# Optimization experiments

Measured on AMD Instinct MI355X. Metric: run time of the kernel, lower is better.

## Reference

```python
import jax, jax.numpy as jnp
import numpy as np

N = 48
K = 16
COLS = N - K  # 32
B = 65536
FEAT = K * COLS + COLS * COLS + K * K + min(K, COLS)  # 1808


def setup_inputs() -> dict:
    key = jax.random.key(0)
    ks = jax.random.split(key, 9)
    def lin(kw, fan_in, fan_out):
        bound = 1.0 / np.sqrt(fan_in)
        return jax.random.uniform(kw, (fan_in, fan_out), jnp.float32, -bound, bound)
    x = jax.random.normal(ks[0], (B, K * COLS), dtype=jnp.float32)
    W1 = lin(ks[1], FEAT, 256); b1 = jnp.zeros((256,), jnp.float32)
    W2 = lin(ks[2], 256, 128);  b2 = jnp.zeros((128,), jnp.float32)
    W3 = lin(ks[3], 128, 64);   b3 = jnp.zeros((64,), jnp.float32)
    W4 = lin(ks[4], 64, 1);     b4 = jnp.zeros((1,), jnp.float32)
    return {"x": x, "W1": W1, "b1": b1, "W2": W2, "b2": b2,
            "W3": W3, "b3": b3, "W4": W4, "b4": b4}


def reference(x, W1, b1, W2, b2, W3, b3, W4, b4):
    Bn = x.shape[0]
    P = x.reshape(Bn, K, COLS)                      # [B,k,cols]
    gram_cols = jnp.einsum('bki,bkj->bij', P, P)    # P^T P, [B,cols,cols]
    gram_rows = jnp.einsum('bik,bjk->bij', P, P)    # P P^T, [B,k,k]
    svd_vals = jnp.linalg.svd(P, compute_uv=False)  # [B,min(k,cols)]
    feats = jnp.concatenate([
        x,
        gram_cols.reshape(Bn, -1),
        gram_rows.reshape(Bn, -1),
        svd_vals,
    ], axis=1)                                       # [B,1808]
    h = jax.nn.relu(feats @ W1 + b1)
    h = jax.nn.relu(h @ W2 + b2)
    h = jax.nn.relu(h @ W3 + b3)
    return h @ W4 + b4                               # [B,1]
```

## Files before the change

### kernel.cpp

```cpp
#include <hip/hip_runtime.h>
#include <hip/hip_bf16.h>
#include <cstdint>
#include <cstddef>

typedef unsigned short u16;
typedef unsigned int u32;
typedef short short8 __attribute__((ext_vector_type(8)));
typedef short short4v __attribute__((ext_vector_type(4)));
typedef __bf16 bf16x8 __attribute__((ext_vector_type(8)));
typedef float v4f __attribute__((ext_vector_type(4)));
typedef float v16f __attribute__((ext_vector_type(16)));

#define NSAMP 65536
#define FEAT_PAD 1824


__device__ __forceinline__ u16 f2bf(float f) {
  union { float f; u32 u; } v; v.f = f;
  u32 r = (v.u + 0x7FFFu + ((v.u >> 16) & 1u)) >> 16;
  return (u16)r;
}
__device__ __forceinline__ float bf2f(u16 h) {
  union { u32 u; float f; } v; v.u = ((u32)h) << 16;
  return v.f;
}

__device__ __forceinline__ v4f mfma16(short8 a, short8 b, v4f c) {
  return __builtin_amdgcn_mfma_f32_16x16x32_bf16(
      __builtin_bit_cast(bf16x8, a), __builtin_bit_cast(bf16x8, b), c, 0, 0, 0);
}
__device__ __forceinline__ v16f mfma32(short8 a, short8 b, v16f c) {
  return __builtin_amdgcn_mfma_f32_32x32x16_bf16(
      __builtin_bit_cast(bf16x8, a), __builtin_bit_cast(bf16x8, b), c, 0, 0, 0);
}

typedef __attribute__((address_space(1))) const void* gas_ptr;
typedef __attribute__((address_space(3))) void* las_ptr;
__device__ __forceinline__ void gl_lds16(const void* g, void* l) {
  __builtin_amdgcn_global_load_lds((gas_ptr)g, (las_ptr)l, 16, 0, 0);
}

__global__ void prep_kernel(const float* __restrict__ W1, const float* __restrict__ W2,
                            const float* __restrict__ W3,
                            u16* __restrict__ w1t, u16* __restrict__ w2t, u16* __restrict__ w3t) {
  int idx = blockIdx.x * 256 + threadIdx.x;
  if (idx < 256 * FEAT_PAD) {
    int n = idx / FEAT_PAD, kp = idx % FEAT_PAD;
    int k;
    if (kp < 512) {
      k = kp;
    } else if (kp < 1536) {
      int t = kp - 512, ln = t >> 4, rr = t & 15;
      int jj = ln & 31, q2 = ln >> 5;
      int i = (rr & 3) + 8 * (rr >> 2) + 4 * q2;
      k = 512 + i * 32 + jj;
    } else if (kp < 1792) {
      int t = kp - 1536, ln = t >> 2, rr = t & 3;
      int jj = ln & 15;
      int i = (ln >> 4) * 4 + rr;
      k = 1536 + i * 16 + jj;
    } else {
      k = kp;
    }
    size_t addr = (size_t)(n >> 4) * 29184 + (kp >> 3) * 128 + (n & 15) * 8 + (kp & 7);
    w1t[addr] = (kp < 1808) ? f2bf(W1[(size_t)k * 256 + n]) : (u16)0;
  }
  if (idx < 128 * 256) {
    int n = idx / 256, k = idx % 256;
    size_t addr = (size_t)(n >> 4) * 4096 + (k >> 3) * 128 + (n & 15) * 8 + (k & 7);
    w2t[addr] = f2bf(W2[k * 128 + n]);
  }
  if (idx < 64 * 128) {
    int n = idx / 128, k = idx % 128;
    size_t addr = (size_t)(n >> 4) * 2048 + (k >> 3) * 128 + (n & 15) * 8 + (k & 7);
    w3t[addr] = f2bf(W3[k * 64 + n]);
  }
}

__device__ __forceinline__ void svd4(const v4f* aR, u16* tb, int s0, int lane) {
  const int j = lane & 15, bse = lane & 48, q = lane >> 4;
  float a[16];
#pragma unroll
  for (int gi = 0; gi < 4; ++gi)
#pragma unroll
    for (int r = 0; r < 4; ++r) {
      float t0 = __shfl(aR[0][r], gi * 16 + j);
      float t1 = __shfl(aR[1][r], gi * 16 + j);
      float t2 = __shfl(aR[2][r], gi * 16 + j);
      float t3 = __shfl(aR[3][r], gi * 16 + j);
      a[gi * 4 + r] = (q == 0) ? t0 : (q == 1) ? t1 : (q == 2) ? t2 : t3;
    }

  float es[16];
#pragma unroll
  for (int i = 0; i < 16; ++i) es[i] = 0.f;

#pragma unroll
  for (int step = 0; step < 14; ++step) {
    const int i = 15 - step, l = i - 1;
    float xv = a[i];
    float xm = (j <= l) ? xv : 0.f;
    float h = xm * xm;
    h += __shfl_xor(h, 1); h += __shfl_xor(h, 2);
    h += __shfl_xor(h, 4); h += __shfl_xor(h, 8);
    float ul = __shfl(xm, bse + l);
    float sq = sqrtf(h);
    float alpha = (ul >= 0.f) ? -sq : sq;
    float denom = h - ul * alpha;
    float beta = (h > 1e-30f) ? (1.0f / denom) : 0.f;
    float v = (j < l) ? xm : ((j == l) ? (xm - alpha) : 0.f);
    float vv[16], pp[16];
#pragma unroll
    for (int m = 0; m < 16; ++m) vv[m] = (m < i) ? __shfl(v, bse + m) : 0.f;
    float p = 0.f;
#pragma unroll
    for (int m = 0; m < 16; ++m) if (m < i) p = fmaf(a[m], vv[m], p);
    p *= beta;
#pragma unroll
    for (int m = 0; m < 16; ++m) pp[m] = (m <= i) ? __shfl(p, bse + m) : 0.f;
    float Ks = 0.f;
#pragma unroll
    for (int m = 0; m < 16; ++m) if (m < i) Ks = fmaf(pp[m], vv[m], Ks);
    Ks *= 0.5f * beta;
    float wsc = p - Ks * v;
#pragma unroll
    for (int m = 0; m <= 15; ++m) {
      if (m <= i) {
        float wm = pp[m] - Ks * vv[m];
        a[m] -= vv[m] * wsc + wm * v;
      }
    }
    es[i] = alpha;
  }
  es[1] = __shfl(a[1], bse + 0);

  float dsel = a[0];
#pragma unroll
  for (int m = 1; m < 16; ++m) dsel = (j == m) ? a[m] : dsel;
  float dd[16];
#pragma unroll
  for (int m = 0; m < 16; ++m) dd[m] = __shfl(dsel, bse + m);
  float e2a[16];
  e2a[0] = 0.f;
#pragma unroll
  for (int k = 1; k < 16; ++k) e2a[k] = es[k] * es[k] + 1e-30f;
  float dmax = dd[0], emax = 0.f;
#pragma unroll
  for (int m = 1; m < 16; ++m) dmax = fmaxf(dmax, dd[m]);
#pragma unroll
  for (int k = 1; k < 16; ++k) emax = fmaxf(emax, fabsf(es[k]));
  float lo = 0.f, hi = dmax + 2.f * emax + 1e-6f;
#pragma unroll 1
  for (int iter = 0; iter < 15; ++iter) {
    float mid = 0.5f * (lo + hi);
    float qq = dd[0] - mid;
    int cnt = (qq < 0.f) ? 1 : 0;
#pragma unroll
    for (int k = 1; k < 16; ++k) {
      qq = dd[k] - mid - e2a[k] * __builtin_amdgcn_rcpf(qq);
      cnt += (qq < 0.f) ? 1 : 0;
    }
    if (cnt > j) hi = mid; else lo = mid;
  }
  float lam = 0.5f * (lo + hi);
  int t = 15 - j;
  int s = s0 + q;
  tb[(size_t)(224 + (t >> 3)) * 128 + (s & 15) * 8 + (t & 7)] = f2bf(sqrtf(fmaxf(lam, 0.f)));
}

__global__ __launch_bounds__(256) void feat_kernel(const float* __restrict__ x,
                                                   u16* __restrict__ feats) {
  const int lane = threadIdx.x & 63;
  const int wv = threadIdx.x >> 6;
  const int wid = blockIdx.x;
  const int l15 = lane & 15, l31 = lane & 31, q4 = lane >> 4, q2 = lane >> 5;
  const int pbase = l15 * 32 + q4 * 8;
  u16* tb = feats + (size_t)wid * 29184;

  short8 sx[4], sc0[4], sc1[4];
  short4v sr4[4];
  v4f aR[4];
#pragma unroll
  for (int r8 = 0; r8 < 4; ++r8) {
    const int s = wid * 16 + wv * 4 + r8;
    const float* xs = x + (size_t)s * 512;
    float4 p0 = *(const float4*)(xs + pbase);
    float4 p1 = *(const float4*)(xs + pbase + 4);
    float t[8];
#pragma unroll
    for (int j = 0; j < 8; ++j) t[j] = xs[(q2 * 8 + j) * 32 + l31];

    short8 fp, ft;
    fp[0] = (short)f2bf(p0.x); fp[1] = (short)f2bf(p0.y);
    fp[2] = (short)f2bf(p0.z); fp[3] = (short)f2bf(p0.w);
    fp[4] = (short)f2bf(p1.x); fp[5] = (short)f2bf(p1.y);
    fp[6] = (short)f2bf(p1.z); fp[7] = (short)f2bf(p1.w);
#pragma unroll
    for (int j = 0; j < 8; ++j) ft[j] = (short)f2bf(t[j]);

    v4f accR; v16f accC;
#pragma unroll
    for (int r = 0; r < 4; ++r) accR[r] = 0.f;
#pragma unroll
    for (int r = 0; r < 16; ++r) accC[r] = 0.f;
    accR = mfma16(fp, fp, accR);
    accC = mfma32(ft, ft, accC);

    sx[r8] = fp;
#pragma unroll
    for (int r = 0; r < 8; ++r) { sc0[r8][r] = (short)f2bf(accC[r]); sc1[r8][r] = (short)f2bf(accC[r + 8]); }
#pragma unroll
    for (int r = 0; r < 4; ++r) sr4[r8][r] = (short)f2bf(accR[r]);
    aR[r8] = accR;
  }

  const int ho = wv * 4;
#pragma unroll
  for (int r8 = 0; r8 < 4; ++r8)
    *(short8*)(tb + (l15 * 4 + q4) * 128 + (ho + r8) * 8) = sx[r8];
#pragma unroll
  for (int r8 = 0; r8 < 4; ++r8)
    *(short8*)(tb + (64 + lane * 2) * 128 + (ho + r8) * 8) = sc0[r8];
#pragma unroll
  for (int r8 = 0; r8 < 4; ++r8)
    *(short8*)(tb + (65 + lane * 2) * 128 + (ho + r8) * 8) = sc1[r8];
#pragma unroll
  for (int r8 = 0; r8 < 4; ++r8)
    *(short4v*)(tb + (192 + (lane >> 1)) * 128 + (lane & 1) * 4 + (ho + r8) * 8) = sr4[r8];

  if (wv == 3 && lane < 32) {
    short8 z;
#pragma unroll
    for (int j = 0; j < 8; ++j) z[j] = 0;
    *(short8*)(tb + 226 * 128 + lane * 8) = z;
  }

  svd4(aR, tb, wid * 16 + ho, lane);
}

__global__ __launch_bounds__(256, 2) void gemm1_kernel(const u16* __restrict__ feats,
                                                       const u16* __restrict__ w1t,
                                                       const float* __restrict__ b1,
                                                       u16* __restrict__ h1) {
  __shared__ __align__(16) u16 At[8 * 512];
  __shared__ __align__(16) u16 Bt[16 * 512];
  const int tid = threadIdx.x, lane = tid & 63, wv = tid >> 6;
  const int l15 = lane & 15, q4 = lane >> 4;
  const int m0 = blockIdx.x * 128;
  const int wm = (wv & 1) * 64, wn = (wv >> 1) * 128;

  const u16* gA[2]; u16* lA[2];
#pragma unroll
  for (int j = 0; j < 2; ++j) {
    int i = wv * 2 + j;
    gA[j] = feats + (size_t)((m0 >> 4) + i) * 29184 + lane * 8;
    lA[j] = At + i * 512;
  }
  const u16* gB[4]; u16* lB[4];
#pragma unroll
  for (int j = 0; j < 4; ++j) {
    int i = wv * 4 + j;
    gB[j] = w1t + (size_t)i * 29184 + lane * 8;
    lB[j] = Bt + i * 512;
  }

  v4f acc[4][8];
#pragma unroll
  for (int mt = 0; mt < 4; ++mt)
#pragma unroll
    for (int nt = 0; nt < 8; ++nt)
#pragma unroll
      for (int r = 0; r < 4; ++r) acc[mt][nt][r] = 0.f;

  for (int k0 = 0; k0 < FEAT_PAD; k0 += 32) {
    const int go = (k0 >> 3) * 128;
#pragma unroll
    for (int j = 0; j < 2; ++j) gl_lds16(gA[j] + go, lA[j]);
#pragma unroll
    for (int j = 0; j < 4; ++j) gl_lds16(gB[j] + go, lB[j]);
    __syncthreads();

    short8 af[4], bfr[8];
#pragma unroll
    for (int mt = 0; mt < 4; ++mt)
      af[mt] = *(const short8*)(At + ((wv & 1) * 4 + mt) * 512 + q4 * 128 + l15 * 8);
#pragma unroll
    for (int nt = 0; nt < 8; ++nt)
      bfr[nt] = *(const short8*)(Bt + ((wv >> 1) * 8 + nt) * 512 + q4 * 128 + l15 * 8);
#pragma unroll
    for (int mt = 0; mt < 4; ++mt)
#pragma unroll
      for (int nt = 0; nt < 8; ++nt)
        acc[mt][nt] = mfma16(af[mt], bfr[nt], acc[mt][nt]);
    __syncthreads();
  }

#pragma unroll
  for (int mt = 0; mt < 4; ++mt)
#pragma unroll
    for (int nt = 0; nt < 8; ++nt) {
      int col = wn + nt * 16 + l15;
      float bias = b1[col];
#pragma unroll
      for (int r = 0; r < 4; ++r) {
        int row = m0 + wm + mt * 16 + q4 * 4 + r;
        h1[(size_t)row * 256 + col] = f2bf(fmaxf(acc[mt][nt][r] + bias, 0.f));
      }
    }
}

__global__ __launch_bounds__(256, 2) void gemm23_kernel(
    const u16* __restrict__ h1, const u16* __restrict__ w2t, const float* __restrict__ b2,
    const u16* __restrict__ w3t, const float* __restrict__ b3,
    const float* __restrict__ w4, const float* __restrict__ b4, float* __restrict__ out) {
  __shared__ __align__(16) u16 H2[128 * 136];
  const int tid = threadIdx.x, lane = tid & 63, wv = tid >> 6;
  const int l15 = lane & 15, q4 = lane >> 4;
  const int m0 = blockIdx.x * 128;

  const u16* pA[2];
#pragma unroll
  for (int mt = 0; mt < 2; ++mt)
    pA[mt] = h1 + (size_t)(m0 + wv * 32 + mt * 16 + l15) * 256 + q4 * 8;
  const u16* pB[8];
#pragma unroll
  for (int nt = 0; nt < 8; ++nt)
    pB[nt] = w2t + (size_t)nt * 4096 + q4 * 128 + l15 * 8;

  v4f acc[2][8];
#pragma unroll
  for (int mt = 0; mt < 2; ++mt)
#pragma unroll
    for (int nt = 0; nt < 8; ++nt)
#pragma unroll
      for (int r = 0; r < 4; ++r) acc[mt][nt][r] = 0.f;

#pragma unroll
  for (int kk = 0; kk < 8; ++kk) {
    short8 af[2], bfr[8];
#pragma unroll
    for (int mt = 0; mt < 2; ++mt) af[mt] = *(const short8*)(pA[mt] + kk * 32);
#pragma unroll
    for (int nt = 0; nt < 8; ++nt) bfr[nt] = *(const short8*)(pB[nt] + kk * 512);
#pragma unroll
    for (int mt = 0; mt < 2; ++mt)
#pragma unroll
      for (int nt = 0; nt < 8; ++nt)
        acc[mt][nt] = mfma16(af[mt], bfr[nt], acc[mt][nt]);
  }

#pragma unroll
  for (int mt = 0; mt < 2; ++mt)
#pragma unroll
    for (int nt = 0; nt < 8; ++nt) {
      int c = nt * 16 + l15;
      float bias = b2[c];
#pragma unroll
      for (int r = 0; r < 4; ++r) {
        int rl = wv * 32 + mt * 16 + q4 * 4 + r;
        H2[rl * 136 + c] = f2bf(fmaxf(acc[mt][nt][r] + bias, 0.f));
      }
    }

  v4f acc2[2][4];
#pragma unroll
  for (int mt = 0; mt < 2; ++mt)
#pragma unroll
    for (int nt = 0; nt < 4; ++nt)
#pragma unroll
      for (int r = 0; r < 4; ++r) acc2[mt][nt][r] = 0.f;
#pragma unroll
  for (int kk = 0; kk < 4; ++kk) {
    short8 af2[2], bf2v[4];
#pragma unroll
    for (int mt = 0; mt < 2; ++mt)
      af2[mt] = *(const short8*)(H2 + (wv * 32 + mt * 16 + l15) * 136 + kk * 32 + q4 * 8);
#pragma unroll
    for (int nt = 0; nt < 4; ++nt)
      bf2v[nt] = *(const short8*)(w3t + (size_t)nt * 2048 + (kk * 4 + q4) * 128 + l15 * 8);
#pragma unroll
    for (int mt = 0; mt < 2; ++mt)
#pragma unroll
      for (int nt = 0; nt < 4; ++nt)
        acc2[mt][nt] = mfma16(af2[mt], bf2v[nt], acc2[mt][nt]);
  }

  float b4v = b4[0];
#pragma unroll
  for (int mt = 0; mt < 2; ++mt)
#pragma unroll
    for (int r = 0; r < 4; ++r) {
      float p = 0.f;
#pragma unroll
      for (int nt = 0; nt < 4; ++nt) {
        int c = nt * 16 + l15;
        float h3 = fmaxf(acc2[mt][nt][r] + b3[c], 0.f);
        p += h3 * w4[c];
      }
      p += __shfl_xor(p, 1);
      p += __shfl_xor(p, 2);
      p += __shfl_xor(p, 4);
      p += __shfl_xor(p, 8);
      if (l15 == 0) {
        int row = m0 + wv * 32 + mt * 16 + q4 * 4 + r;
        out[row] = p + b4v;
      }
    }
}

extern "C" void kernel_launch(void* const* d_in, const int* in_sizes, int n_in,
                              void* d_out, int out_size, void* d_ws, size_t ws_size,
                              hipStream_t stream) {
  const float* x  = (const float*)d_in[0];
  const float* W1 = (const float*)d_in[1];
  const float* b1 = (const float*)d_in[2];
  const float* W2 = (const float*)d_in[3];
  const float* b2 = (const float*)d_in[4];
  const float* W3 = (const float*)d_in[5];
  const float* b3 = (const float*)d_in[6];
  const float* W4 = (const float*)d_in[7];
  const float* b4 = (const float*)d_in[8];
  float* out = (float*)d_out;

  char* ws = (char*)d_ws;
  u16* feats = (u16*)ws;
  u16* h1    = (u16*)(ws + 239075328ull);
  u16* w1t   = (u16*)(ws + 239075328ull + 33554432ull);
  u16* w2t   = (u16*)(ws + 239075328ull + 33554432ull + 933888ull);
  u16* w3t   = (u16*)(ws + 239075328ull + 33554432ull + 933888ull + 65536ull);

  prep_kernel<<<1824, 256, 0, stream>>>(W1, W2, W3, w1t, w2t, w3t);
  feat_kernel<<<4096, 256, 0, stream>>>(x, feats);
  gemm1_kernel<<<512, 256, 0, stream>>>(feats, w1t, b1, h1);
  gemm23_kernel<<<512, 256, 0, stream>>>(h1, w2t, b2, w3t, b3, W4, b4, out);
}
```

Baseline: 419.2 us.

## Fuse layer-1 GEMM with layers 2-4 via shared-memory h1 staging

Merges gemm1 and gemm23 into a single mlp_kernel. The ReLU'd layer-1 output is written to shared memory in two 64-row halves and consumed in place by the layer-2/3/4 MFMAs, so the 32 MB bf16 h1 round-trip through global memory and one kernel launch go away. Shared memory per block grows to about 50 KB, which may limit occupancy. The extra barriers and serial half loop also leave the accumulator registers live during the tail.

```diff
diff --git a/kernel.cpp b/kernel.cpp
--- a/kernel.cpp
+++ b/kernel.cpp
@@ -238,12 +238,17 @@
   svd4(aR, tb, wid * 16 + ho, lane);
 }
 
-__global__ __launch_bounds__(256, 2) void gemm1_kernel(const u16* __restrict__ feats,
-                                                       const u16* __restrict__ w1t,
-                                                       const float* __restrict__ b1,
-                                                       u16* __restrict__ h1) {
-  __shared__ __align__(16) u16 At[8 * 512];
-  __shared__ __align__(16) u16 Bt[16 * 512];
+__global__ __launch_bounds__(256, 2) void mlp_kernel(
+    const u16* __restrict__ feats, const u16* __restrict__ w1t, const float* __restrict__ b1,
+    const u16* __restrict__ w2t, const float* __restrict__ b2,
+    const u16* __restrict__ w3t, const float* __restrict__ b3,
+    const float* __restrict__ w4, const float* __restrict__ b4, float* __restrict__ out) {
+  __shared__ __align__(16) char sm[51200];
+  u16* At  = (u16*)sm;
+  u16* Bt  = (u16*)(sm + 8192);
+  u16* h1s = (u16*)sm;
+  u16* H2  = (u16*)(sm + 33792);
+
   const int tid = threadIdx.x, lane = tid & 63, wv = tid >> 6;
   const int l15 = lane & 15, q4 = lane >> 4;
   const int m0 = blockIdx.x * 128;
@@ -295,106 +300,71 @@
     __syncthreads();
   }
 
-#pragma unroll
-  for (int mt = 0; mt < 4; ++mt)
-#pragma unroll
-    for (int nt = 0; nt < 8; ++nt) {
-      int col = wn + nt * 16 + l15;
-      float bias = b1[col];
-#pragma unroll
-      for (int r = 0; r < 4; ++r) {
-        int row = m0 + wm + mt * 16 + q4 * 4 + r;
-        h1[(size_t)row * 256 + col] = f2bf(fmaxf(acc[mt][nt][r] + bias, 0.f));
+  const float b4v = b4[0];
+#pragma unroll 1
+  for (int h = 0; h < 2; ++h) {
+    __syncthreads();
+    if ((wv & 1) == h) {
+#pragma unroll
+      for (int mt = 0; mt < 4; ++mt)
+#pragma unroll
+        for (int nt = 0; nt < 8; ++nt) {
+          int col = wn + nt * 16 + l15;
+          float bias = b1[col];
+#pragma unroll
+          for (int r = 0; r < 4; ++r)
+            h1s[(mt * 16 + q4 * 4 + r) * 264 + col] = f2bf(fmaxf(acc[mt][nt][r] + bias, 0.f));
+        }
+    }
+    __syncthreads();
+
+    v4f a2[8];
+#pragma unroll
+    for (int nt = 0; nt < 8; ++nt)
+#pragma unroll
+      for (int r = 0; r < 4; ++r) a2[nt][r] = 0.f;
+#pragma unroll
+    for (int kk = 0; kk < 8; ++kk) {
+      short8 af2 = *(const short8*)(h1s + (wv * 16 + l15) * 264 + kk * 32 + q4 * 8);
+#pragma unroll
+      for (int nt = 0; nt < 8; ++nt) {
+        short8 bfr2 = *(const short8*)(w2t + (size_t)nt * 4096 + (kk * 4 + q4) * 128 + l15 * 8);
+        a2[nt] = mfma16(af2, bfr2, a2[nt]);
       }
     }
-}
-
-__global__ __launch_bounds__(256, 2) void gemm23_kernel(
-    const u16* __restrict__ h1, const u16* __restrict__ w2t, const float* __restrict__ b2,
-    const u16* __restrict__ w3t, const float* __restrict__ b3,
-    const float* __restrict__ w4, const float* __restrict__ b4, float* __restrict__ out) {
-  __shared__ __align__(16) u16 H2[128 * 136];
-  const int tid = threadIdx.x, lane = tid & 63, wv = tid >> 6;
-  const int l15 = lane & 15, q4 = lane >> 4;
-  const int m0 = blockIdx.x * 128;
-
-  const u16* pA[2];
-#pragma unroll
-  for (int mt = 0; mt < 2; ++mt)
-    pA[mt] = h1 + (size_t)(m0 + wv * 32 + mt * 16 + l15) * 256 + q4 * 8;
-  const u16* pB[8];
-#pragma unroll
-  for (int nt = 0; nt < 8; ++nt)
-    pB[nt] = w2t + (size_t)nt * 4096 + q4 * 128 + l15 * 8;
-
-  v4f acc[2][8];
-#pragma unroll
-  for (int mt = 0; mt < 2; ++mt)
-#pragma unroll
-    for (int nt = 0; nt < 8; ++nt)
-#pragma unroll
-      for (int r = 0; r < 4; ++r) acc[mt][nt][r] = 0.f;
-
-#pragma unroll
-  for (int kk = 0; kk < 8; ++kk) {
-    short8 af[2], bfr[8];
-#pragma unroll
-    for (int mt = 0; mt < 2; ++mt) af[mt] = *(const short8*)(pA[mt] + kk * 32);
-#pragma unroll
-    for (int nt = 0; nt < 8; ++nt) bfr[nt] = *(const short8*)(pB[nt] + kk * 512);
-#pragma unroll
-    for (int mt = 0; mt < 2; ++mt)
-#pragma unroll
-      for (int nt = 0; nt < 8; ++nt)
-        acc[mt][nt] = mfma16(af[mt], bfr[nt], acc[mt][nt]);
-  }
-
-#pragma unroll
-  for (int mt = 0; mt < 2; ++mt)
+
+    u16* myH2 = H2 + wv * 16 * 136;
 #pragma unroll
     for (int nt = 0; nt < 8; ++nt) {
       int c = nt * 16 + l15;
       float bias = b2[c];
 #pragma unroll
-      for (int r = 0; r < 4; ++r) {
-        int rl = wv * 32 + mt * 16 + q4 * 4 + r;
-        H2[rl * 136 + c] = f2bf(fmaxf(acc[mt][nt][r] + bias, 0.f));
+      for (int r = 0; r < 4; ++r)
+        myH2[(q4 * 4 + r) * 136 + c] = f2bf(fmaxf(a2[nt][r] + bias, 0.f));
+    }
+
+    v4f a3[4];
+#pragma unroll
+    for (int nt = 0; nt < 4; ++nt)
+#pragma unroll
+      for (int r = 0; r < 4; ++r) a3[nt][r] = 0.f;
+#pragma unroll
+    for (int kk = 0; kk < 4; ++kk) {
+      short8 af3 = *(const short8*)(myH2 + l15 * 136 + kk * 32 + q4 * 8);
+#pragma unroll
+      for (int nt = 0; nt < 4; ++nt) {
+        short8 bfr3 = *(const short8*)(w3t + (size_t)nt * 2048 + (kk * 4 + q4) * 128 + l15 * 8);
+        a3[nt] = mfma16(af3, bfr3, a3[nt]);
       }
     }
 
-  v4f acc2[2][4];
-#pragma unroll
-  for (int mt = 0; mt < 2; ++mt)
-#pragma unroll
-    for (int nt = 0; nt < 4; ++nt)
-#pragma unroll
-      for (int r = 0; r < 4; ++r) acc2[mt][nt][r] = 0.f;
-#pragma unroll
-  for (int kk = 0; kk < 4; ++kk) {
-    short8 af2[2], bf2v[4];
-#pragma unroll
-    for (int mt = 0; mt < 2; ++mt)
-      af2[mt] = *(const short8*)(H2 + (wv * 32 + mt * 16 + l15) * 136 + kk * 32 + q4 * 8);
-#pragma unroll
-    for (int nt = 0; nt < 4; ++nt)
-      bf2v[nt] = *(const short8*)(w3t + (size_t)nt * 2048 + (kk * 4 + q4) * 128 + l15 * 8);
-#pragma unroll
-    for (int mt = 0; mt < 2; ++mt)
-#pragma unroll
-      for (int nt = 0; nt < 4; ++nt)
-        acc2[mt][nt] = mfma16(af2[mt], bf2v[nt], acc2[mt][nt]);
-  }
-
-  float b4v = b4[0];
-#pragma unroll
-  for (int mt = 0; mt < 2; ++mt)
 #pragma unroll
     for (int r = 0; r < 4; ++r) {
       float p = 0.f;
 #pragma unroll
       for (int nt = 0; nt < 4; ++nt) {
         int c = nt * 16 + l15;
-        float h3 = fmaxf(acc2[mt][nt][r] + b3[c], 0.f);
+        float h3 = fmaxf(a3[nt][r] + b3[c], 0.f);
         p += h3 * w4[c];
       }
       p += __shfl_xor(p, 1);
@@ -402,10 +372,11 @@
       p += __shfl_xor(p, 4);
       p += __shfl_xor(p, 8);
       if (l15 == 0) {
-        int row = m0 + wv * 32 + mt * 16 + q4 * 4 + r;
+        int row = m0 + h * 64 + wv * 16 + q4 * 4 + r;
         out[row] = p + b4v;
       }
     }
+  }
 }
 
 extern "C" void kernel_launch(void* const* d_in, const int* in_sizes, int n_in,
@@ -424,13 +395,11 @@
 
   char* ws = (char*)d_ws;
   u16* feats = (u16*)ws;
-  u16* h1    = (u16*)(ws + 239075328ull);
-  u16* w1t   = (u16*)(ws + 239075328ull + 33554432ull);
-  u16* w2t   = (u16*)(ws + 239075328ull + 33554432ull + 933888ull);
-  u16* w3t   = (u16*)(ws + 239075328ull + 33554432ull + 933888ull + 65536ull);
+  u16* w1t   = (u16*)(ws + 239075328ull);
+  u16* w2t   = (u16*)(ws + 239075328ull + 933888ull);
+  u16* w3t   = (u16*)(ws + 239075328ull + 933888ull + 65536ull);
 
   prep_kernel<<<1824, 256, 0, stream>>>(W1, W2, W3, w1t, w2t, w3t);
   feat_kernel<<<4096, 256, 0, stream>>>(x, feats);
-  gemm1_kernel<<<512, 256, 0, stream>>>(feats, w1t, b1, h1);
-  gemm23_kernel<<<512, 256, 0, stream>>>(h1, w2t, b2, w3t, b3, W4, b4, out);
-}
+  mlp_kernel<<<512, 256, 0, stream>>>(feats, w1t, b1, w2t, b2, w3t, b3, W4, b4, out);
+}
```

Measured after the change: 502.7 us. 1.2x slower.
